# Performance work log

Measured on AMD Instinct MI355X. Metric: run time of the kernel, lower is better.

## Reference

```python
import jax, jax.numpy as jnp
import numpy as np
import math

D = 2048
H = 32
HKV = 8
HD = D // H
ROPE_BASE = 10000.0


def _rope_cache(T, hd, base=ROPE_BASE):
    theta = 1.0 / base ** (jnp.arange(0, hd, 2, dtype=jnp.float32) / hd)  # [hd//2]
    t = jnp.arange(T, dtype=jnp.float32)
    freqs = t[:, None] * theta[None, :]  # [T, hd//2]
    return jnp.cos(freqs), jnp.sin(freqs)


def _apply_rope(x, cos, sin):
    # x: [B, H, T, HD]; interleaved-pair rotation
    B, Hh, T, hd = x.shape
    x_ = x.reshape(B, Hh, T, hd // 2, 2)
    x1, x2 = x_[..., 0], x_[..., 1]
    c = cos[None, None, :, :]
    s = sin[None, None, :, :]
    rx1 = x1 * c - x2 * s
    rx2 = x1 * s + x2 * c
    return jnp.stack([rx1, rx2], axis=-1).reshape(B, Hh, T, hd)


def setup_inputs() -> dict:
    key = jax.random.key(0)
    ks = jax.random.split(key, 5)
    B, T = 1, 2048
    sc = 0.02
    return {
        "x": jax.random.normal(ks[0], (B, T, D), dtype=jnp.float32),
        "wq": jax.random.normal(ks[1], (D, D), dtype=jnp.float32) * sc,
        "wk": jax.random.normal(ks[2], (HKV * HD, D), dtype=jnp.float32) * sc,
        "wv": jax.random.normal(ks[3], (HKV * HD, D), dtype=jnp.float32) * sc,
        "wo": jax.random.normal(ks[4], (D, D), dtype=jnp.float32) * sc,
    }


def reference(x, wq, wk, wv, wo):
    B, T, _ = x.shape
    q = (x @ wq.T).reshape(B, T, H, HD).transpose(0, 2, 1, 3)      # [B,H,T,HD]
    k = (x @ wk.T).reshape(B, T, HKV, HD).transpose(0, 2, 1, 3)    # [B,HKV,T,HD]
    v = (x @ wv.T).reshape(B, T, HKV, HD).transpose(0, 2, 1, 3)

    cos, sin = _rope_cache(T, HD)
    q = _apply_rope(q, cos, sin)
    k = _apply_rope(k, cos, sin)

    rep = H // HKV
    k = jnp.repeat(k, rep, axis=1)  # repeat_interleave over head dim
    v = jnp.repeat(v, rep, axis=1)

    scores = jnp.einsum("bhtd,bhsd->bhts", q, k) / math.sqrt(HD)
    mask = jnp.triu(jnp.full((T, T), -jnp.inf, dtype=scores.dtype), k=1)
    scores = scores + mask[None, None, :, :]
    attn = jax.nn.softmax(scores, axis=-1)

    y = jnp.einsum("bhts,bhsd->bhtd", attn, v)
    y = y.transpose(0, 2, 1, 3).reshape(B, T, D)
    return y @ wo.T
```

## Files before the change

### kernel.cpp

```cpp
#include <hip/hip_runtime.h>
#include <hip/hip_bf16.h>
#include <cstdint>
#include <cstddef>

#define TT 2048
#define DDIM 2048
#define NH 32
#define NKV 8
#define HDIM 64

typedef __attribute__((ext_vector_type(8))) short bf16x8;
typedef __attribute__((ext_vector_type(4))) float f32x4;
typedef __attribute__((ext_vector_type(16))) float f32x16;

__device__ __forceinline__ unsigned short f2bf(float f) {
  unsigned u = __float_as_uint(f);
  unsigned r = 0x7FFFu + ((u >> 16) & 1u);
  return (unsigned short)((u + r) >> 16);
}
__device__ __forceinline__ float bf2f(unsigned short u) {
  return __uint_as_float((unsigned)u << 16);
}

__device__ __forceinline__ void gl_lds16(const void* g, void* l) {
  __builtin_amdgcn_global_load_lds(
      (const __attribute__((address_space(1))) void*)g,
      (__attribute__((address_space(3))) void*)l, 16, 0, 0);
}

__device__ __forceinline__ unsigned pkbf(float lo, float hi) {
  unsigned r;
  asm("v_cvt_pk_bf16_f32 %0, %1, %2" : "=v"(r) : "v"(lo), "v"(hi));
  return r;
}
__device__ __forceinline__ void swap32(unsigned& dst, unsigned& src) {
  asm volatile("v_permlane32_swap_b32 %0, %1" : "+v"(dst), "+v"(src));
}
union W4 { unsigned w[4]; bf16x8 v; };

__global__ __launch_bounds__(256)
void cast5_kernel(const float* __restrict__ x, const float* __restrict__ wq,
                  const float* __restrict__ wk, const float* __restrict__ wv,
                  const float* __restrict__ wo,
                  unsigned short* __restrict__ xb, unsigned short* __restrict__ wqb,
                  unsigned short* __restrict__ wkb, unsigned short* __restrict__ wvb,
                  unsigned short* __restrict__ wob) {
  int i = blockIdx.x * 256 + threadIdx.x;
  const float* s; unsigned short* d; int off;
  if (i < 1048576)      { s = x;  d = xb;  off = i; }
  else if (i < 2097152) { s = wq; d = wqb; off = i - 1048576; }
  else if (i < 2359296) { s = wk; d = wkb; off = i - 2097152; }
  else if (i < 2621440) { s = wv; d = wvb; off = i - 2359296; }
  else                  { s = wo; d = wob; off = i - 2621440; }
  float4 f = reinterpret_cast<const float4*>(s)[off];
  ushort4 o;
  o.x = f2bf(f.x); o.y = f2bf(f.y); o.z = f2bf(f.z); o.w = f2bf(f.w);
  reinterpret_cast<ushort4*>(d)[off] = o;
}

__device__ __forceinline__ void gemm64_body(
    const unsigned short* __restrict__ A, const unsigned short* __restrict__ B,
    int K, size_t arow, size_t brow,
    unsigned short (*As)[64 * 64], unsigned short (*Bs)[128 * 64],
    f32x4 (&acc)[2][4]) {
  const int tid = threadIdx.x;
  const int wave = tid >> 6, lane = tid & 63;
  const int wm = wave >> 1, wn = wave & 1;
  const int lr = lane & 15;
  const int gb = lane >> 4;
  const int srow = lane >> 3;
  const int scol = (((lane & 7) ^ srow) << 3);

#define G64_STAGE(buf, k0)                                                       \
  {                                                                              \
    for (int i = 0; i < 2; ++i) {                                                \
      int blk = wave * 2 + i;                                                    \
      int r = blk * 8 + srow;                                                    \
      gl_lds16(A + arow + (size_t)r * K + (k0) + scol, &As[buf][blk * 8 * 64]);  \
    }                                                                            \
    for (int i = 0; i < 4; ++i) {                                                \
      int blk = wave * 4 + i;                                                    \
      int r = blk * 8 + srow;                                                    \
      gl_lds16(B + brow + (size_t)r * K + (k0) + scol, &Bs[buf][blk * 8 * 64]);  \
    }                                                                            \
  }

  const int nt = K >> 6;
  G64_STAGE(0, 0)
  __syncthreads();
  int cur = 0;
  for (int t = 0; t < nt; ++t) {
    if (t + 1 < nt) { G64_STAGE(cur ^ 1, (t + 1) << 6) }

    bf16x8 af[2][2], bfr[2][4];
    for (int mi = 0; mi < 2; ++mi) {
      int row = wm * 32 + mi * 16 + lr, sw = row & 7;
      af[0][mi] = *reinterpret_cast<const bf16x8*>(&As[cur][row * 64 + ((gb ^ sw) << 3)]);
      af[1][mi] = *reinterpret_cast<const bf16x8*>(&As[cur][row * 64 + (((4 + gb) ^ sw) << 3)]);
    }
    for (int ni = 0; ni < 4; ++ni) {
      int row = wn * 64 + ni * 16 + lr, sw = row & 7;
      bfr[0][ni] = *reinterpret_cast<const bf16x8*>(&Bs[cur][row * 64 + ((gb ^ sw) << 3)]);
      bfr[1][ni] = *reinterpret_cast<const bf16x8*>(&Bs[cur][row * 64 + (((4 + gb) ^ sw) << 3)]);
    }
    __builtin_amdgcn_s_setprio(1);
    for (int kk = 0; kk < 2; ++kk)
      for (int mi = 0; mi < 2; ++mi)
        for (int ni = 0; ni < 4; ++ni)
          acc[mi][ni] = __builtin_amdgcn_mfma_f32_16x16x32_bf16(af[kk][mi], bfr[kk][ni], acc[mi][ni], 0, 0, 0);
    __builtin_amdgcn_s_setprio(0);
    __syncthreads();
    cur ^= 1;
  }
#undef G64_STAGE
}

__global__ __launch_bounds__(256, 3)
void qkv_fused_kernel(const unsigned short* __restrict__ xb,
                      const unsigned short* __restrict__ wqb,
                      const unsigned short* __restrict__ wkb,
                      const unsigned short* __restrict__ wvb,
                      unsigned short* __restrict__ qhb,
                      unsigned short* __restrict__ khb,
                      unsigned short* __restrict__ vtb) {
  __shared__ __align__(16) unsigned short As[2][64 * 64];
  __shared__ __align__(16) unsigned short Bs[2][128 * 64];
  const int bn = blockIdx.y;
  const unsigned short* B; int n0, mode;
  if (bn < 16)      { B = wqb; n0 = bn;      mode = 0; }
  else if (bn < 20) { B = wkb; n0 = bn - 16; mode = 1; }
  else              { B = wvb; n0 = bn - 20; mode = 2; }

  f32x4 acc[2][4];
  for (int i = 0; i < 2; ++i)
    for (int j = 0; j < 4; ++j)
      acc[i][j] = (f32x4){0.f, 0.f, 0.f, 0.f};

  gemm64_body(xb, B, 2048, (size_t)(blockIdx.x * 64) * 2048,
              (size_t)(n0 * 128) * 2048, As, Bs, acc);

  const int tid = threadIdx.x;
  const int wave = tid >> 6, lane = tid & 63;
  const int wm = wave >> 1, wn = wave & 1;
  const int lr = lane & 15;

  if (mode == 2) {
#pragma unroll
    for (int mi = 0; mi < 2; ++mi)
#pragma unroll
      for (int ni = 0; ni < 4; ++ni) {
        int n = n0 * 128 + wn * 64 + ni * 16 + lr;
        int tb = blockIdx.x * 64 + wm * 32 + mi * 16 + (lane >> 4) * 4;
        ushort4 u;
        u.x = f2bf(acc[mi][ni][0]); u.y = f2bf(acc[mi][ni][1]);
        u.z = f2bf(acc[mi][ni][2]); u.w = f2bf(acc[mi][ni][3]);
        *reinterpret_cast<ushort4*>(&vtb[(size_t)n * TT + tb]) = u;
      }
  } else {
    unsigned short* dst = (mode == 0) ? qhb : khb;
    const float scale = (mode == 0) ? 0.125f : 1.0f;
#pragma unroll
    for (int mi = 0; mi < 2; ++mi)
#pragma unroll
      for (int ni = 0; ni < 4; ++ni) {
        int n = n0 * 128 + wn * 64 + ni * 16 + lr;
        int hh = n >> 6, d = n & 63, ii = d >> 1;
        float theta = exp2f(-(float)(2 * ii) * (13.287712379549449f / 64.0f));
        int tb = blockIdx.x * 64 + wm * 32 + mi * 16 + (lane >> 4) * 4;
#pragma unroll
        for (int r = 0; r < 4; ++r) {
          float self = acc[mi][ni][r];
          float part = __shfl_xor(self, 1);
          float sn, cs;
          __sincosf((float)(tb + r) * theta, &sn, &cs);
          float val = (d & 1) ? (part * sn + self * cs) : (self * cs - part * sn);
          dst[((size_t)hh * TT + tb + r) * HDIM + d] = f2bf(val * scale);
        }
      }
  }
}

__global__ __launch_bounds__(256, 3)
void out_gemm_kernel(const unsigned short* __restrict__ yb,
                     const unsigned short* __restrict__ wob,
                     float* __restrict__ out) {
  __shared__ __align__(16) unsigned short As[2][64 * 64];
  __shared__ __align__(16) unsigned short Bs[2][128 * 64];
  f32x4 acc[2][4];
  for (int i = 0; i < 2; ++i)
    for (int j = 0; j < 4; ++j)
      acc[i][j] = (f32x4){0.f, 0.f, 0.f, 0.f};

  gemm64_body(yb, wob, 2048, (size_t)(blockIdx.x * 64) * 2048,
              (size_t)(blockIdx.y * 128) * 2048, As, Bs, acc);

  const int tid = threadIdx.x;
  const int wave = tid >> 6, lane = tid & 63;
  const int wm = wave >> 1, wn = wave & 1;
  const int lr = lane & 15;
#pragma unroll
  for (int mi = 0; mi < 2; ++mi)
#pragma unroll
    for (int ni = 0; ni < 4; ++ni) {
      int col = blockIdx.y * 128 + wn * 64 + ni * 16 + lr;
      int rbase = blockIdx.x * 64 + wm * 32 + mi * 16 + (lane >> 4) * 4;
#pragma unroll
      for (int r = 0; r < 4; ++r)
        out[(size_t)(rbase + r) * DDIM + col] = acc[mi][ni][r];
    }
}

__global__ __launch_bounds__(256)
void attn_kernel(const unsigned short* __restrict__ qh,
                 const unsigned short* __restrict__ kh,
                 const unsigned short* __restrict__ vt,
                 unsigned short* __restrict__ po,
                 float* __restrict__ pm, float* __restrict__ pl) {
  __shared__ __align__(16) unsigned short Ks[2][64 * 64];
  __shared__ __align__(16) unsigned short Vts[2][64 * 64];
  const int kvg = blockIdx.x;
  const int by = blockIdx.y;
  const int qt = 63 - (by >> 1);
  const int par = by & 1;
  const int tid = threadIdx.x, wave = tid >> 6, lane = tid & 63;
  const int h = kvg * 4 + wave;
  const int qc = lane & 31, hi = lane >> 5;
  const int srow = lane >> 3;
  const int scol = (((lane & 7) ^ srow) << 3);

  bf16x8 qa[4];
  {
    const unsigned short* qrow = qh + ((size_t)h * TT + qt * 32 + qc) * HDIM + hi * 8;
#pragma unroll
    for (int ks = 0; ks < 4; ++ks)
      qa[ks] = *reinterpret_cast<const bf16x8*>(qrow + ks * 16);
  }

  f32x16 oA, oB;
#pragma unroll
  for (int r = 0; r < 16; ++r) { oA[r] = 0.f; oB[r] = 0.f; }
  float m_r = -1e30f, l_r = 0.f;

  const int njb = (qt >> 1) + 1;
  const int cnt = (njb - par + 1) >> 1;

#define A_STAGE(buf, jbx) do {                                                        \
    for (int i = 0; i < 2; ++i) {                                                     \
      int blk = wave * 2 + i;                                                         \
      int rr = blk * 8 + srow;                                                        \
      gl_lds16(kh + ((size_t)kvg * TT + (size_t)(jbx) * 64 + rr) * HDIM + scol,       \
               &Ks[buf][blk * 8 * 64]);                                               \
      gl_lds16(vt + ((size_t)(kvg * HDIM + rr)) * TT + (size_t)(jbx) * 64 + scol,     \
               &Vts[buf][blk * 8 * 64]);                                              \
    } } while (0)

  if (cnt > 0) {
    A_STAGE(0, par);
    __syncthreads();
    int cur = 0;

    for (int it = 0; it < cnt; ++it) {
      const int jb = par + 2 * it;
      if (it + 1 < cnt) A_STAGE(cur ^ 1, jb + 2);
      const bool diag = (jb == njb - 1);
      const bool hasB = (!diag) || (qt & 1);

      f32x16 stA, stB;
#pragma unroll
      for (int r = 0; r < 16; ++r) { stA[r] = 0.f; stB[r] = 0.f; }
      __builtin_amdgcn_s_setprio(1);
#pragma unroll
      for (int ks = 0; ks < 4; ++ks) {
        int row = qc, g = 2 * ks + hi;
        bf16x8 kf = *reinterpret_cast<const bf16x8*>(&Ks[cur][row * 64 + ((g ^ (row & 7)) << 3)]);
        stA = __builtin_amdgcn_mfma_f32_32x32x16_bf16(kf, qa[ks], stA, 0, 0, 0);
      }
      if (hasB) {
#pragma unroll
        for (int ks = 0; ks < 4; ++ks) {
          int row = 32 + qc, g = 2 * ks + hi;
          bf16x8 kf = *reinterpret_cast<const bf16x8*>(&Ks[cur][row * 64 + ((g ^ (row & 7)) << 3)]);
          stB = __builtin_amdgcn_mfma_f32_32x32x16_bf16(kf, qa[ks], stB, 0, 0, 0);
        }
      }
      __builtin_amdgcn_s_setprio(0);

      if (diag) {
        if (qt & 1) {
#pragma unroll
          for (int r = 0; r < 16; ++r) {
            int jloc = (r & 3) + 8 * (r >> 2) + 4 * hi;
            stB[r] = (jloc > qc) ? -1e30f : stB[r];
          }
        } else {
#pragma unroll
          for (int r = 0; r < 16; ++r) {
            int jloc = (r & 3) + 8 * (r >> 2) + 4 * hi;
            stA[r] = (jloc > qc) ? -1e30f : stA[r];
          }
        }
      }

      float pmx = stA[0];
#pragma unroll
      for (int r = 1; r < 16; ++r) pmx = fmaxf(pmx, stA[r]);
      if (hasB) {
#pragma unroll
        for (int r = 0; r < 16; ++r) pmx = fmaxf(pmx, stB[r]);
      }
      pmx = fmaxf(pmx, __shfl_xor(pmx, 32));
      if (!__all(pmx <= m_r + 8.f)) {
        float mn = fmaxf(m_r, pmx);
        float al = __expf(m_r - mn);
        m_r = mn; l_r *= al;
#pragma unroll
        for (int r = 0; r < 16; ++r) {
          int qrow = (r & 3) + 8 * (r >> 2) + 4 * hi;
          float alr = __shfl(al, qrow);
          oA[r] *= alr; oB[r] *= alr;
        }
      }
      float sum = 0.f;
#pragma unroll
      for (int r = 0; r < 16; ++r) { stA[r] = __expf(stA[r] - m_r); sum += stA[r]; }
      if (hasB) {
#pragma unroll
        for (int r = 0; r < 16; ++r) { stB[r] = __expf(stB[r] - m_r); sum += stB[r]; }
      }
      sum += __shfl_xor(sum, 32);
      l_r += sum;

      W4 pf0, pf1, pf2, pf3;
#define REPACK(F0, F1, S)                                                   \
      F0.w[0] = pkbf(S[0], S[1]);  F0.w[1] = pkbf(S[2], S[3]);              \
      F0.w[2] = pkbf(S[4], S[5]);  F0.w[3] = pkbf(S[6], S[7]);              \
      swap32(F0.w[0], F0.w[2]);    swap32(F0.w[1], F0.w[3]);                \
      F1.w[0] = pkbf(S[8], S[9]);  F1.w[1] = pkbf(S[10], S[11]);            \
      F1.w[2] = pkbf(S[12], S[13]); F1.w[3] = pkbf(S[14], S[15]);           \
      swap32(F1.w[0], F1.w[2]);    swap32(F1.w[1], F1.w[3]);
      REPACK(pf0, pf1, stA)
      if (hasB) { REPACK(pf2, pf3, stB) }
#undef REPACK

      {
        const unsigned short* Vb = &Vts[cur][0];
        int r0 = qc, r1 = 32 + qc;
        int s0 = r0 & 7, s1 = r1 & 7;
        bf16x8 b;
        __builtin_amdgcn_s_setprio(1);
        b = *reinterpret_cast<const bf16x8*>(Vb + r0 * 64 + (((0 + hi) ^ s0) << 3));
        oA = __builtin_amdgcn_mfma_f32_32x32x16_bf16(pf0.v, b, oA, 0, 0, 0);
        b = *reinterpret_cast<const bf16x8*>(Vb + r1 * 64 + (((0 + hi) ^ s1) << 3));
        oB = __builtin_amdgcn_mfma_f32_32x32x16_bf16(pf0.v, b, oB, 0, 0, 0);
        b = *reinterpret_cast<const bf16x8*>(Vb + r0 * 64 + (((2 + hi) ^ s0) << 3));
        oA = __builtin_amdgcn_mfma_f32_32x32x16_bf16(pf1.v, b, oA, 0, 0, 0);
        b = *reinterpret_cast<const bf16x8*>(Vb + r1 * 64 + (((2 + hi) ^ s1) << 3));
        oB = __builtin_amdgcn_mfma_f32_32x32x16_bf16(pf1.v, b, oB, 0, 0, 0);
        if (hasB) {
          b = *reinterpret_cast<const bf16x8*>(Vb + r0 * 64 + (((4 + hi) ^ s0) << 3));
          oA = __builtin_amdgcn_mfma_f32_32x32x16_bf16(pf2.v, b, oA, 0, 0, 0);
          b = *reinterpret_cast<const bf16x8*>(Vb + r1 * 64 + (((4 + hi) ^ s1) << 3));
          oB = __builtin_amdgcn_mfma_f32_32x32x16_bf16(pf2.v, b, oB, 0, 0, 0);
          b = *reinterpret_cast<const bf16x8*>(Vb + r0 * 64 + (((6 + hi) ^ s0) << 3));
          oA = __builtin_amdgcn_mfma_f32_32x32x16_bf16(pf3.v, b, oA, 0, 0, 0);
          b = *reinterpret_cast<const bf16x8*>(Vb + r1 * 64 + (((6 + hi) ^ s1) << 3));
          oB = __builtin_amdgcn_mfma_f32_32x32x16_bf16(pf3.v, b, oB, 0, 0, 0);
        }
        __builtin_amdgcn_s_setprio(0);
      }
      __syncthreads();
      cur ^= 1;
    }
  }
#undef A_STAGE

#pragma unroll
  for (int r = 0; r < 16; ++r) {
    int qrow = (r & 3) + 8 * (r >> 2) + 4 * hi;
    size_t base = (((size_t)par * NH + h) * TT + qt * 32 + qrow) * HDIM + qc;
    po[base] = f2bf(oA[r]);
    po[base + 32] = f2bf(oB[r]);
  }
  if (hi == 0) {
    size_t idx = ((size_t)par * NH + h) * TT + qt * 32 + qc;
    pm[idx] = m_r;
    pl[idx] = l_r;
  }
}

__global__ __launch_bounds__(256)
void attn_merge_kernel(const unsigned short* __restrict__ po,
                       const float* __restrict__ pm, const float* __restrict__ pl,
                       unsigned short* __restrict__ y) {
  int idx = blockIdx.x * 256 + threadIdx.x;
  int d = idx & 63;
  int row = idx >> 6;
  int h = row >> 11, t = row & (TT - 1);
  const size_t P = (size_t)NH * TT * HDIM;
  float m0 = pm[row], m1 = pm[NH * TT + row];
  float l0 = pl[row], l1 = pl[NH * TT + row];
  float M = fmaxf(m0, m1);
  float w0 = __expf(m0 - M), w1 = __expf(m1 - M);
  float o0 = bf2f(po[(size_t)row * HDIM + d]);
  float o1 = bf2f(po[P + (size_t)row * HDIM + d]);
  float val = (w0 * o0 + w1 * o1) / (w0 * l0 + w1 * l1);
  y[(size_t)t * DDIM + h * HDIM + d] = f2bf(val);
}

extern "C" void kernel_launch(void* const* d_in, const int* in_sizes, int n_in,
                              void* d_out, int out_size, void* d_ws, size_t ws_size,
                              hipStream_t stream) {
  const float* x  = (const float*)d_in[0];
  const float* wq = (const float*)d_in[1];
  const float* wk = (const float*)d_in[2];
  const float* wv = (const float*)d_in[3];
  const float* wo = (const float*)d_in[4];
  float* out = (float*)d_out;
  char* ws = (char*)d_ws;

  unsigned short* xb  = (unsigned short*)(ws + (size_t)0);
  unsigned short* wqb = (unsigned short*)(ws + ((size_t)8  << 20));
  unsigned short* wkb = (unsigned short*)(ws + ((size_t)16 << 20));
  unsigned short* wvb = (unsigned short*)(ws + ((size_t)18 << 20));
  unsigned short* wob = (unsigned short*)(ws + ((size_t)20 << 20));
  unsigned short* po  = (unsigned short*)(ws + ((size_t)28 << 20));
  float*          pm  = (float*)(ws + ((size_t)44 << 20));
  float*          pl  = (float*)(ws + ((size_t)44 << 20) + ((size_t)512 << 10));
  unsigned short* qhb = (unsigned short*)(ws + ((size_t)52 << 20));
  unsigned short* khb = (unsigned short*)(ws + ((size_t)60 << 20));
  unsigned short* vtb = (unsigned short*)(ws + ((size_t)62 << 20));
  unsigned short* yb  = (unsigned short*)(ws + ((size_t)64 << 20));

  cast5_kernel<<<14336, 256, 0, stream>>>(x, wq, wk, wv, wo, xb, wqb, wkb, wvb, wob);

  qkv_fused_kernel<<<dim3(32, 24), 256, 0, stream>>>(xb, wqb, wkb, wvb, qhb, khb, vtb);

  attn_kernel<<<dim3(8, 128), 256, 0, stream>>>(qhb, khb, vtb, po, pm, pl);
  attn_merge_kernel<<<16384, 256, 0, stream>>>(po, pm, pl, yb);

  out_gemm_kernel<<<dim3(32, 16), 256, 0, stream>>>(yb, wob, out);
}
```

Measured before the change: 120.8 us.

## Split attention KV range four ways and use exp2-based softmax

Increases the KV split from two to four partitions so the attention grid has more blocks. The merge kernel now combines four partials with vectorized loads. Log2(e) is folded into the Q scale so softmax can use exp2, the lazy rescale threshold is raised, and K-fragment loads are interleaved with the QK MFMAs. The extra partitions add more partial-output traffic and a heavier merge, with workspace regions reused to hold them.

Measured after the change: 136.7 us. +13.1%, slower.

```diff
diff --git a/kernel.cpp b/kernel.cpp
--- a/kernel.cpp
+++ b/kernel.cpp
@@ -158,7 +158,7 @@
       }
   } else {
     unsigned short* dst = (mode == 0) ? qhb : khb;
-    const float scale = (mode == 0) ? 0.125f : 1.0f;
+    const float scale = (mode == 0) ? 0.18033688011112042f : 1.0f;
 #pragma unroll
     for (int mi = 0; mi < 2; ++mi)
 #pragma unroll
@@ -214,14 +214,15 @@
 void attn_kernel(const unsigned short* __restrict__ qh,
                  const unsigned short* __restrict__ kh,
                  const unsigned short* __restrict__ vt,
-                 unsigned short* __restrict__ po,
+                 unsigned short* __restrict__ po012,
+                 unsigned short* __restrict__ po3,
                  float* __restrict__ pm, float* __restrict__ pl) {
   __shared__ __align__(16) unsigned short Ks[2][64 * 64];
   __shared__ __align__(16) unsigned short Vts[2][64 * 64];
   const int kvg = blockIdx.x;
   const int by = blockIdx.y;
-  const int qt = 63 - (by >> 1);
-  const int par = by & 1;
+  const int qt = 63 - (by >> 2);
+  const int par = by & 3;
   const int tid = threadIdx.x, wave = tid >> 6, lane = tid & 63;
   const int h = kvg * 4 + wave;
   const int qc = lane & 31, hi = lane >> 5;
@@ -242,45 +243,49 @@
   float m_r = -1e30f, l_r = 0.f;
 
   const int njb = (qt >> 1) + 1;
-  const int cnt = (njb - par + 1) >> 1;
-
-#define A_STAGE(buf, jbx) do {                                                        \
-    for (int i = 0; i < 2; ++i) {                                                     \
-      int blk = wave * 2 + i;                                                         \
-      int rr = blk * 8 + srow;                                                        \
-      gl_lds16(kh + ((size_t)kvg * TT + (size_t)(jbx) * 64 + rr) * HDIM + scol,       \
-               &Ks[buf][blk * 8 * 64]);                                               \
-      gl_lds16(vt + ((size_t)(kvg * HDIM + rr)) * TT + (size_t)(jbx) * 64 + scol,     \
-               &Vts[buf][blk * 8 * 64]);                                              \
-    } } while (0)
+  const int cnt = (njb > par) ? ((njb - par + 3) >> 2) : 0;
+
+  const unsigned short* kbase = kh + (size_t)kvg * TT * HDIM + scol;
+  const unsigned short* vbase = vt + (size_t)kvg * HDIM * TT + scol;
+  const int rrA = (wave * 2) * 8 + srow;
+  const int rrB = (wave * 2 + 1) * 8 + srow;
+
+#define A_STAGE(buf, KO, VO) do {                                   \
+    gl_lds16(kbase + (KO) + (size_t)rrA * HDIM, &Ks[buf][(wave * 2) * 512]);     \
+    gl_lds16(kbase + (KO) + (size_t)rrB * HDIM, &Ks[buf][(wave * 2 + 1) * 512]); \
+    gl_lds16(vbase + (VO) + (size_t)rrA * TT, &Vts[buf][(wave * 2) * 512]);      \
+    gl_lds16(vbase + (VO) + (size_t)rrB * TT, &Vts[buf][(wave * 2 + 1) * 512]);  \
+  } while (0)
 
   if (cnt > 0) {
-    A_STAGE(0, par);
+    size_t koff = (size_t)par * 64 * HDIM;
+    size_t voff = (size_t)par * 64;
+    A_STAGE(0, koff, voff);
     __syncthreads();
     int cur = 0;
 
     for (int it = 0; it < cnt; ++it) {
-      const int jb = par + 2 * it;
-      if (it + 1 < cnt) A_STAGE(cur ^ 1, jb + 2);
+      const int jb = par + 4 * it;
+      if (it + 1 < cnt) A_STAGE(cur ^ 1, koff + 4 * 64 * HDIM, voff + 4 * 64);
       const bool diag = (jb == njb - 1);
       const bool hasB = (!diag) || (qt & 1);
 
       f32x16 stA, stB;
 #pragma unroll
       for (int r = 0; r < 16; ++r) { stA[r] = 0.f; stB[r] = 0.f; }
+      const int swq = (qc & 7) << 3;
       __builtin_amdgcn_s_setprio(1);
 #pragma unroll
       for (int ks = 0; ks < 4; ++ks) {
-        int row = qc, g = 2 * ks + hi;
-        bf16x8 kf = *reinterpret_cast<const bf16x8*>(&Ks[cur][row * 64 + ((g ^ (row & 7)) << 3)]);
-        stA = __builtin_amdgcn_mfma_f32_32x32x16_bf16(kf, qa[ks], stA, 0, 0, 0);
-      }
-      if (hasB) {
-#pragma unroll
-        for (int ks = 0; ks < 4; ++ks) {
-          int row = 32 + qc, g = 2 * ks + hi;
-          bf16x8 kf = *reinterpret_cast<const bf16x8*>(&Ks[cur][row * 64 + ((g ^ (row & 7)) << 3)]);
-          stB = __builtin_amdgcn_mfma_f32_32x32x16_bf16(kf, qa[ks], stB, 0, 0, 0);
+        int g = (2 * ks + hi) << 3;
+        int off = qc * 64 + (g ^ swq);
+        bf16x8 ka = *reinterpret_cast<const bf16x8*>(&Ks[cur][off]);
+        if (hasB) {
+          bf16x8 kb = *reinterpret_cast<const bf16x8*>(&Ks[cur][off + 2048]);
+          stA = __builtin_amdgcn_mfma_f32_32x32x16_bf16(ka, qa[ks], stA, 0, 0, 0);
+          stB = __builtin_amdgcn_mfma_f32_32x32x16_bf16(kb, qa[ks], stB, 0, 0, 0);
+        } else {
+          stA = __builtin_amdgcn_mfma_f32_32x32x16_bf16(ka, qa[ks], stA, 0, 0, 0);
         }
       }
       __builtin_amdgcn_s_setprio(0);
@@ -301,17 +306,18 @@
         }
       }
 
-      float pmx = stA[0];
-#pragma unroll
-      for (int r = 1; r < 16; ++r) pmx = fmaxf(pmx, stA[r]);
+      float pmx = fmaxf(fmaxf(stA[0], stA[1]), stA[2]);
+#pragma unroll
+      for (int r = 3; r < 15; r += 2) pmx = fmaxf(fmaxf(pmx, stA[r]), stA[r + 1]);
+      pmx = fmaxf(pmx, stA[15]);
       if (hasB) {
 #pragma unroll
-        for (int r = 0; r < 16; ++r) pmx = fmaxf(pmx, stB[r]);
+        for (int r = 0; r < 16; r += 2) pmx = fmaxf(fmaxf(pmx, stB[r]), stB[r + 1]);
       }
       pmx = fmaxf(pmx, __shfl_xor(pmx, 32));
-      if (!__all(pmx <= m_r + 8.f)) {
+      if (!__all(pmx <= m_r + 12.f)) {
         float mn = fmaxf(m_r, pmx);
-        float al = __expf(m_r - mn);
+        float al = exp2f(m_r - mn);
         m_r = mn; l_r *= al;
 #pragma unroll
         for (int r = 0; r < 16; ++r) {
@@ -322,10 +328,10 @@
       }
       float sum = 0.f;
 #pragma unroll
-      for (int r = 0; r < 16; ++r) { stA[r] = __expf(stA[r] - m_r); sum += stA[r]; }
+      for (int r = 0; r < 16; ++r) { stA[r] = exp2f(stA[r] - m_r); sum += stA[r]; }
       if (hasB) {
 #pragma unroll
-        for (int r = 0; r < 16; ++r) { stB[r] = __expf(stB[r] - m_r); sum += stB[r]; }
+        for (int r = 0; r < 16; ++r) { stB[r] = exp2f(stB[r] - m_r); sum += stB[r]; }
       }
       sum += __shfl_xor(sum, 32);
       l_r += sum;
@@ -344,40 +350,43 @@
 
       {
         const unsigned short* Vb = &Vts[cur][0];
-        int r0 = qc, r1 = 32 + qc;
-        int s0 = r0 & 7, s1 = r1 & 7;
+        const int sv = (qc & 7) << 3;
+        const int vb0 = qc * 64;
         bf16x8 b;
         __builtin_amdgcn_s_setprio(1);
-        b = *reinterpret_cast<const bf16x8*>(Vb + r0 * 64 + (((0 + hi) ^ s0) << 3));
+        b = *reinterpret_cast<const bf16x8*>(Vb + vb0 + ((hi << 3) ^ sv));
         oA = __builtin_amdgcn_mfma_f32_32x32x16_bf16(pf0.v, b, oA, 0, 0, 0);
-        b = *reinterpret_cast<const bf16x8*>(Vb + r1 * 64 + (((0 + hi) ^ s1) << 3));
+        b = *reinterpret_cast<const bf16x8*>(Vb + vb0 + 2048 + ((hi << 3) ^ sv));
         oB = __builtin_amdgcn_mfma_f32_32x32x16_bf16(pf0.v, b, oB, 0, 0, 0);
-        b = *reinterpret_cast<const bf16x8*>(Vb + r0 * 64 + (((2 + hi) ^ s0) << 3));
+        b = *reinterpret_cast<const bf16x8*>(Vb + vb0 + (((2 + hi) << 3) ^ sv));
         oA = __builtin_amdgcn_mfma_f32_32x32x16_bf16(pf1.v, b, oA, 0, 0, 0);
-        b = *reinterpret_cast<const bf16x8*>(Vb + r1 * 64 + (((2 + hi) ^ s1) << 3));
+        b = *reinterpret_cast<const bf16x8*>(Vb + vb0 + 2048 + (((2 + hi) << 3) ^ sv));
         oB = __builtin_amdgcn_mfma_f32_32x32x16_bf16(pf1.v, b, oB, 0, 0, 0);
         if (hasB) {
-          b = *reinterpret_cast<const bf16x8*>(Vb + r0 * 64 + (((4 + hi) ^ s0) << 3));
+          b = *reinterpret_cast<const bf16x8*>(Vb + vb0 + (((4 + hi) << 3) ^ sv));
           oA = __builtin_amdgcn_mfma_f32_32x32x16_bf16(pf2.v, b, oA, 0, 0, 0);
-          b = *reinterpret_cast<const bf16x8*>(Vb + r1 * 64 + (((4 + hi) ^ s1) << 3));
+          b = *reinterpret_cast<const bf16x8*>(Vb + vb0 + 2048 + (((4 + hi) << 3) ^ sv));
           oB = __builtin_amdgcn_mfma_f32_32x32x16_bf16(pf2.v, b, oB, 0, 0, 0);
-          b = *reinterpret_cast<const bf16x8*>(Vb + r0 * 64 + (((6 + hi) ^ s0) << 3));
+          b = *reinterpret_cast<const bf16x8*>(Vb + vb0 + (((6 + hi) << 3) ^ sv));
           oA = __builtin_amdgcn_mfma_f32_32x32x16_bf16(pf3.v, b, oA, 0, 0, 0);
-          b = *reinterpret_cast<const bf16x8*>(Vb + r1 * 64 + (((6 + hi) ^ s1) << 3));
+          b = *reinterpret_cast<const bf16x8*>(Vb + vb0 + 2048 + (((6 + hi) << 3) ^ sv));
           oB = __builtin_amdgcn_mfma_f32_32x32x16_bf16(pf3.v, b, oB, 0, 0, 0);
         }
         __builtin_amdgcn_s_setprio(0);
       }
       __syncthreads();
       cur ^= 1;
+      koff += 4 * 64 * HDIM;
+      voff += 4 * 64;
     }
   }
 #undef A_STAGE
 
+  unsigned short* po = (par < 3) ? (po012 + (size_t)par * (NH * TT * HDIM)) : po3;
 #pragma unroll
   for (int r = 0; r < 16; ++r) {
     int qrow = (r & 3) + 8 * (r >> 2) + 4 * hi;
-    size_t base = (((size_t)par * NH + h) * TT + qt * 32 + qrow) * HDIM + qc;
+    size_t base = ((size_t)h * TT + qt * 32 + qrow) * HDIM + qc;
     po[base] = f2bf(oA[r]);
     po[base + 32] = f2bf(oB[r]);
   }
@@ -389,22 +398,37 @@
 }
 
 __global__ __launch_bounds__(256)
-void attn_merge_kernel(const unsigned short* __restrict__ po,
+void attn_merge_kernel(const unsigned short* __restrict__ po012,
+                       const unsigned short* __restrict__ po3,
                        const float* __restrict__ pm, const float* __restrict__ pl,
                        unsigned short* __restrict__ y) {
   int idx = blockIdx.x * 256 + threadIdx.x;
-  int d = idx & 63;
-  int row = idx >> 6;
+  int row = idx >> 4;
+  int d0 = (idx & 15) << 2;
   int h = row >> 11, t = row & (TT - 1);
   const size_t P = (size_t)NH * TT * HDIM;
-  float m0 = pm[row], m1 = pm[NH * TT + row];
-  float l0 = pl[row], l1 = pl[NH * TT + row];
-  float M = fmaxf(m0, m1);
-  float w0 = __expf(m0 - M), w1 = __expf(m1 - M);
-  float o0 = bf2f(po[(size_t)row * HDIM + d]);
-  float o1 = bf2f(po[P + (size_t)row * HDIM + d]);
-  float val = (w0 * o0 + w1 * o1) / (w0 * l0 + w1 * l1);
-  y[(size_t)t * DDIM + h * HDIM + d] = f2bf(val);
+  const int NT = NH * TT;
+
+  float m[4], l[4];
+#pragma unroll
+  for (int p = 0; p < 4; ++p) { m[p] = pm[p * NT + row]; l[p] = pl[p * NT + row]; }
+  float M = fmaxf(fmaxf(m[0], m[1]), fmaxf(m[2], m[3]));
+  float acc[4] = {0.f, 0.f, 0.f, 0.f};
+  float L = 0.f;
+#pragma unroll
+  for (int p = 0; p < 4; ++p) {
+    float w = exp2f(m[p] - M);
+    L += w * l[p];
+    const unsigned short* po = (p < 3) ? (po012 + (size_t)p * P) : po3;
+    ushort4 u = *reinterpret_cast<const ushort4*>(&po[(size_t)row * HDIM + d0]);
+    acc[0] += w * bf2f(u.x); acc[1] += w * bf2f(u.y);
+    acc[2] += w * bf2f(u.z); acc[3] += w * bf2f(u.w);
+  }
+  float inv = 1.0f / L;
+  ushort4 o;
+  o.x = f2bf(acc[0] * inv); o.y = f2bf(acc[1] * inv);
+  o.z = f2bf(acc[2] * inv); o.w = f2bf(acc[3] * inv);
+  *reinterpret_cast<ushort4*>(&y[(size_t)t * DDIM + h * HDIM + d0]) = o;
 }
 
 extern "C" void kernel_launch(void* const* d_in, const int* in_sizes, int n_in,
@@ -423,9 +447,10 @@
   unsigned short* wkb = (unsigned short*)(ws + ((size_t)16 << 20));
   unsigned short* wvb = (unsigned short*)(ws + ((size_t)18 << 20));
   unsigned short* wob = (unsigned short*)(ws + ((size_t)20 << 20));
-  unsigned short* po  = (unsigned short*)(ws + ((size_t)28 << 20));
-  float*          pm  = (float*)(ws + ((size_t)44 << 20));
-  float*          pl  = (float*)(ws + ((size_t)44 << 20) + ((size_t)512 << 10));
+  unsigned short* po012 = (unsigned short*)(ws + ((size_t)28 << 20));
+  unsigned short* po3 = (unsigned short*)(ws + (size_t)0);
+  float*          pm  = (float*)(ws + ((size_t)8 << 20));
+  float*          pl  = (float*)(ws + ((size_t)9 << 20));
   unsigned short* qhb = (unsigned short*)(ws + ((size_t)52 << 20));
   unsigned short* khb = (unsigned short*)(ws + ((size_t)60 << 20));
   unsigned short* vtb = (unsigned short*)(ws + ((size_t)62 << 20));
@@ -435,8 +460,8 @@
 
   qkv_fused_kernel<<<dim3(32, 24), 256, 0, stream>>>(xb, wqb, wkb, wvb, qhb, khb, vtb);
 
-  attn_kernel<<<dim3(8, 128), 256, 0, stream>>>(qhb, khb, vtb, po, pm, pl);
-  attn_merge_kernel<<<16384, 256, 0, stream>>>(po, pm, pl, yb);
+  attn_kernel<<<dim3(8, 256), 256, 0, stream>>>(qhb, khb, vtb, po012, po3, pm, pl);
+  attn_merge_kernel<<<4096, 256, 0, stream>>>(po012, po3, pm, pl, yb);
 
   out_gemm_kernel<<<dim3(32, 16), 256, 0, stream>>>(yb, wob, out);
 }
```
